# Performance work log

Measured on AMD Instinct MI355X. Metric: run time of the kernel, lower is better.

The kernel has to match this reference:

```python
import jax, jax.numpy as jnp
import numpy as np

B, N, C_IN, C_CH = 1, 512, 128, 128

def layer_norm(x, g, b, eps=1e-5):
    mu = jnp.mean(x, axis=-1, keepdims=True)
    var = jnp.var(x, axis=-1, keepdims=True)
    return (x - mu) * jax.lax.rsqrt(var + eps) * g + b

def setup_inputs() -> dict:
    key = jax.random.key(0)
    ks = jax.random.split(key, 16)
    s = 0.02
    # weights stored as [in, out] (torch Linear uses y = x @ W.T + b; we pre-transpose)
    return {
        "z": jax.random.normal(ks[0], (B, N, N, C_IN), jnp.float32),
        "mask": jax.random.randint(ks[1], (B, N, N), 0, 2).astype(bool),
        "g_in": jnp.ones((C_IN,), jnp.float32),
        "b_in": jnp.zeros((C_IN,), jnp.float32),
        "Wa": jax.random.normal(ks[2], (C_IN, C_CH), jnp.float32) * s,
        "ba": jnp.zeros((C_CH,), jnp.float32),
        "Wga": jax.random.normal(ks[3], (C_IN, C_CH), jnp.float32) * s,
        "bga": jax.random.normal(ks[4], (C_CH,), jnp.float32) * s,
        "Wb": jax.random.normal(ks[5], (C_IN, C_CH), jnp.float32) * s,
        "bb": jnp.zeros((C_CH,), jnp.float32),
        "Wgb": jax.random.normal(ks[6], (C_IN, C_CH), jnp.float32) * s,
        "bgb": jax.random.normal(ks[7], (C_CH,), jnp.float32) * s,
        "g_o": jnp.ones((C_CH,), jnp.float32),
        "b_o": jnp.zeros((C_CH,), jnp.float32),
        "Wgo": jax.random.normal(ks[8], (C_IN, C_IN), jnp.float32) * s,
        "bgo": jax.random.normal(ks[9], (C_IN,), jnp.float32) * s,
        "Wo": jax.random.normal(ks[10], (C_CH, C_IN), jnp.float32) * s,
        "bo": jnp.zeros((C_IN,), jnp.float32),
    }

def reference(z, mask, g_in, b_in, Wa, ba, Wga, bga, Wb, bb, Wgb, bgb,
              g_o, b_o, Wgo, bgo, Wo, bo):
    zn = layer_norm(z, g_in, b_in)                                  # [B,N,N,Cin]
    a = jax.nn.sigmoid(zn @ Wga + bga) * (zn @ Wa + ba)             # [B,N,N,Cch]
    b = jax.nn.sigmoid(zn @ Wgb + bgb) * (zn @ Wb + bb)
    m = mask[..., None]                                             # [B,N,N,1]
    a = jnp.where(m, 0.0, a)
    b = jnp.where(m, 0.0, b)
    # axis == 1: k[b,i,j,o] = sum_k a[b,i,k,o] * b[b,j,k,o]
    k = jnp.einsum('biko,bjko->bijo', a, b)
    return jax.nn.sigmoid(zn @ Wgo + bgo) * (layer_norm(k, g_o, b_o) @ Wo + bo)
```

## Files before the change

kernel.cpp:

```cpp
#include <hip/hip_runtime.h>

#define NDIM 512
#define CDIM 128
#define RDIM (NDIM * NDIM)

typedef __attribute__((ext_vector_type(8))) short bf16x8;
typedef __attribute__((ext_vector_type(8))) unsigned short ushort8;
typedef __attribute__((ext_vector_type(4))) float f32x4;

__device__ __forceinline__ float bf2f(unsigned short u) {
  union { unsigned int i; float f; } v; v.i = ((unsigned int)u) << 16; return v.f;
}
__device__ __forceinline__ unsigned short f2bf(float f) {
  union { float f; unsigned int i; } v; v.f = f;
  unsigned int r = v.i + 0x7fffu + ((v.i >> 16) & 1u);
  return (unsigned short)(r >> 16);
}
__device__ __forceinline__ float sigm(float x) { return 1.0f / (1.0f + __expf(-x)); }

__device__ __forceinline__ int sw(int row, int col) {
  return (row << 7) + ((((col >> 3) ^ (row & 7)) << 3) | (col & 7));
}

__global__ __launch_bounds__(256) void k0_prep(
    const float* __restrict__ Wga, const float* __restrict__ Wa,
    const float* __restrict__ Wgb, const float* __restrict__ Wb,
    const float* __restrict__ Wgo, const float* __restrict__ Wo,
    unsigned short* __restrict__ wsF) {
  const float* src;
  switch (blockIdx.x) {
    case 0: src = Wga; break;
    case 1: src = Wa;  break;
    case 2: src = Wgb; break;
    case 3: src = Wb;  break;
    case 4: src = Wgo; break;
    default: src = Wo; break;
  }
  const int t = threadIdx.x;
  unsigned short* dstF = wsF + blockIdx.x * 16384;
  for (int gid = t; gid < 2048; gid += 256) {
    const int fragid = gid >> 6, lane = gid & 63;
    const int kc = fragid >> 3, nf = fragid & 7;
    const int o = nf * 16 + (lane & 15);
    const int c0 = kc * 32 + (lane >> 4) * 8;
#pragma unroll
    for (int j = 0; j < 8; j++) dstF[gid * 8 + j] = f2bf(src[(c0 + j) * CDIM + o]);
  }
}

__device__ __forceinline__ bf16x8 ldfrag(const unsigned short* wf, int slot, int kc,
                                         int nf, int lane) {
  return *((const bf16x8*)(wf + (((slot * 32 + kc * 8 + nf) * 64 + lane) << 3)));
}

__global__ __launch_bounds__(256, 3) void k1_proj(
    const float* __restrict__ z, const int* __restrict__ mask,
    const float* __restrict__ g_in, const float* __restrict__ b_in,
    const float* __restrict__ bga, const float* __restrict__ ba,
    const float* __restrict__ bgb, const float* __restrict__ bb,
    const unsigned short* __restrict__ wf,
    unsigned short* __restrict__ a_t, unsigned short* __restrict__ b_t) {
  __shared__ unsigned short Xs[CDIM * CDIM];
  const int t = threadIdx.x;
  const int lane = t & 63;
  const int w = t >> 6;
  const int l15 = lane & 15, lq = lane >> 4;
  const int row0 = blockIdx.x * 128;

  {
    const int row = t >> 1, hf = t & 1;
    const float4* zp = (const float4*)(z + (size_t)(row0 + row) * CDIM + hf * 64);
    float s = 0.f, s2 = 0.f;
#pragma unroll
    for (int i = 0; i < 16; i++) {
      float4 x = zp[i];
      s += x.x + x.y + x.z + x.w;
      s2 += x.x * x.x + x.y * x.y + x.z * x.z + x.w * x.w;
    }
    s += __shfl_xor(s, 1);
    s2 += __shfl_xor(s2, 1);
    const float mean = s * 0.0078125f;
    const float var = s2 * 0.0078125f - mean * mean;
    const float rs = rsqrtf(var + 1e-5f);
    const float4* gp = (const float4*)(g_in + hf * 64);
    const float4* bp = (const float4*)(b_in + hf * 64);
#pragma unroll 4
    for (int u = 0; u < 8; u++) {
      float4 x0 = zp[2 * u], x1 = zp[2 * u + 1];
      float4 g0 = gp[2 * u], g1 = gp[2 * u + 1];
      float4 c0 = bp[2 * u], c1 = bp[2 * u + 1];
      ushort8 pk;
      pk[0] = f2bf((x0.x - mean) * rs * g0.x + c0.x);
      pk[1] = f2bf((x0.y - mean) * rs * g0.y + c0.y);
      pk[2] = f2bf((x0.z - mean) * rs * g0.z + c0.z);
      pk[3] = f2bf((x0.w - mean) * rs * g0.w + c0.w);
      pk[4] = f2bf((x1.x - mean) * rs * g1.x + c1.x);
      pk[5] = f2bf((x1.y - mean) * rs * g1.y + c1.y);
      pk[6] = f2bf((x1.z - mean) * rs * g1.z + c1.z);
      pk[7] = f2bf((x1.w - mean) * rs * g1.w + c1.w);
      const int su = (hf * 8 + u) ^ (row & 7);
      *((ushort8*)&Xs[(row << 7) + (su << 3)]) = pk;
    }
  }

  unsigned mbits = 0;
#pragma unroll
  for (int ms = 0; ms < 2; ms++)
#pragma unroll
    for (int r = 0; r < 4; r++) {
      const int rl = w * 32 + ms * 16 + (lq << 2) + r;
      if (mask[row0 + rl] != 0) mbits |= 1u << (ms * 4 + r);
    }

  __syncthreads();

  bf16x8 afr[2][4];
#pragma unroll
  for (int ms = 0; ms < 2; ms++) {
    const int m = w * 32 + ms * 16 + l15;
#pragma unroll
    for (int kc = 0; kc < 4; kc++)
      afr[ms][kc] = *((const bf16x8*)&Xs[sw(m, kc * 32 + (lq << 3))]);
  }
  __syncthreads();

  const f32x4 zv = {0.f, 0.f, 0.f, 0.f};

#pragma unroll 1
  for (int pair = 0; pair < 2; pair++) {
    const int sg = pair * 2, sv = pair * 2 + 1;
    const float* bgp = (pair == 0) ? bga : bgb;
    const float* bvp = (pair == 0) ? ba : bb;
#pragma unroll 1
    for (int half = 0; half < 2; half++) {
      f32x4 accg[2][4], accv[2][4];
#pragma unroll
      for (int i = 0; i < 2; i++)
#pragma unroll
        for (int j = 0; j < 4; j++) { accg[i][j] = zv; accv[i][j] = zv; }
#pragma unroll
      for (int kc = 0; kc < 4; kc++) {
#pragma unroll
        for (int nfh = 0; nfh < 4; nfh++) {
          const int fi = half * 4 + nfh;
          bf16x8 bg = ldfrag(wf, sg, kc, fi, lane);
          bf16x8 bv = ldfrag(wf, sv, kc, fi, lane);
          accg[0][nfh] = __builtin_amdgcn_mfma_f32_16x16x32_bf16(afr[0][kc], bg, accg[0][nfh], 0, 0, 0);
          accg[1][nfh] = __builtin_amdgcn_mfma_f32_16x16x32_bf16(afr[1][kc], bg, accg[1][nfh], 0, 0, 0);
          accv[0][nfh] = __builtin_amdgcn_mfma_f32_16x16x32_bf16(afr[0][kc], bv, accv[0][nfh], 0, 0, 0);
          accv[1][nfh] = __builtin_amdgcn_mfma_f32_16x16x32_bf16(afr[1][kc], bv, accv[1][nfh], 0, 0, 0);
        }
      }
#pragma unroll
      for (int ms = 0; ms < 2; ms++)
#pragma unroll
        for (int nfh = 0; nfh < 4; nfh++) {
          const int n = half * 64 + nfh * 16 + l15;
          const float bg = bgp[n], bv = bvp[n];
#pragma unroll
          for (int r = 0; r < 4; r++) {
            const int rl = w * 32 + ms * 16 + (lq << 2) + r;
            float val = sigm(accg[ms][nfh][r] + bg) * (accv[ms][nfh][r] + bv);
            if ((mbits >> (ms * 4 + r)) & 1u) val = 0.f;
            Xs[sw(n, rl)] = f2bf(val);
          }
        }
    }
    __syncthreads();
    unsigned short* dst = (pair == 0) ? a_t : b_t;
    {
      const int o = t >> 1, hf = t & 1;
#pragma unroll
      for (int u = 0; u < 8; u++) {
        const int ru = hf * 8 + u;
        const int su = ru ^ (o & 7);
        uint4 val = *((const uint4*)&Xs[(o << 7) + (su << 3)]);
        *((uint4*)&dst[(size_t)o * RDIM + row0 + ru * 8]) = val;
      }
    }
    __syncthreads();
  }
}

__global__ __launch_bounds__(256) void k2_einsum(
    const unsigned short* __restrict__ a_t, const unsigned short* __restrict__ b_t,
    unsigned short* __restrict__ k_t) {
  __shared__ unsigned short As[128 * 72];
  __shared__ unsigned short Bs[128 * 72];
  const int t = threadIdx.x;
  const int lane = t & 63;
  const int w = t >> 6;
  const int l15 = lane & 15, lq = lane >> 4;
  const int bid = (blockIdx.x & 7) * (2048 >> 3) + (blockIdx.x >> 3);
  const int o = bid >> 4;
  const int tile = bid & 15;
  const int i0 = (tile >> 2) * 128, j0 = (tile & 3) * 128;
  const size_t base = (size_t)o * RDIM;

  f32x4 acc[2][8];
  const f32x4 zv = {0.f, 0.f, 0.f, 0.f};
#pragma unroll
  for (int i = 0; i < 2; i++)
#pragma unroll
    for (int j = 0; j < 8; j++) acc[i][j] = zv;

  const int r = t & 127;
  const int isB = t >> 7;
  const unsigned short* srcp = (isB ? b_t : a_t) + base + (size_t)((isB ? j0 : i0) + r) * NDIM;
  unsigned short* dstp = isB ? &Bs[r * 72] : &As[r * 72];

  for (int k0 = 0; k0 < NDIM; k0 += 64) {
    __syncthreads();
    const uint4* s4 = (const uint4*)(srcp + k0);
#pragma unroll
    for (int u = 0; u < 8; u++) *((uint4*)&dstp[u * 8]) = s4[u];
    __syncthreads();
#pragma unroll
    for (int kc = 0; kc < 2; kc++) {
      const int kk = kc * 32 + (lq << 3);
      bf16x8 a0 = *((const bf16x8*)&As[(w * 32 + l15) * 72 + kk]);
      bf16x8 a1 = *((const bf16x8*)&As[(w * 32 + 16 + l15) * 72 + kk]);
#pragma unroll
      for (int nf = 0; nf < 8; nf++) {
        bf16x8 bfr = *((const bf16x8*)&Bs[(nf * 16 + l15) * 72 + kk]);
        acc[0][nf] = __builtin_amdgcn_mfma_f32_16x16x32_bf16(a0, bfr, acc[0][nf], 0, 0, 0);
        acc[1][nf] = __builtin_amdgcn_mfma_f32_16x16x32_bf16(a1, bfr, acc[1][nf], 0, 0, 0);
      }
    }
  }
#pragma unroll
  for (int ms = 0; ms < 2; ms++)
#pragma unroll
    for (int nf = 0; nf < 8; nf++)
#pragma unroll
      for (int r2 = 0; r2 < 4; r2++) {
        const int mi = i0 + w * 32 + ms * 16 + (lq << 2) + r2;
        const int nj = j0 + nf * 16 + l15;
        k_t[base + (size_t)mi * NDIM + nj] = f2bf(acc[ms][nf][r2]);
      }
}

__global__ __launch_bounds__(256, 2) void k3_final(
    const unsigned short* __restrict__ k_t, const unsigned short* __restrict__ wf,
    const float* __restrict__ z, const float* __restrict__ g_in,
    const float* __restrict__ b_in, const float* __restrict__ g_o,
    const float* __restrict__ b_o, const float* __restrict__ bgo,
    const float* __restrict__ bo, float* __restrict__ out) {
  __shared__ unsigned short Ks[CDIM * CDIM];
  __shared__ unsigned short XN[CDIM * CDIM];
  const int t = threadIdx.x;
  const int lane = t & 63;
  const int w = t >> 6;
  const int l15 = lane & 15, lq = lane >> 4;
  const int row0 = blockIdx.x * 128;

  {
    const int o = t >> 1, hf = t & 1;
    const uint4* src = (const uint4*)(k_t + (size_t)o * RDIM + row0 + hf * 64);
#pragma unroll
    for (int u = 0; u < 8; u++) {
      const int ru = hf * 8 + u;
      const int su = ru ^ (o & 7);
      *((uint4*)&Ks[(o << 7) + (su << 3)]) = src[u];
    }
  }
  {
    const int row = t >> 1, hf = t & 1;
    const float4* zp = (const float4*)(z + (size_t)(row0 + row) * CDIM + hf * 64);
    float s = 0.f, s2 = 0.f;
#pragma unroll
    for (int i = 0; i < 16; i++) {
      float4 x = zp[i];
      s += x.x + x.y + x.z + x.w;
      s2 += x.x * x.x + x.y * x.y + x.z * x.z + x.w * x.w;
    }
    s += __shfl_xor(s, 1);
    s2 += __shfl_xor(s2, 1);
    const float mean = s * 0.0078125f;
    const float var = s2 * 0.0078125f - mean * mean;
    const float rs = rsqrtf(var + 1e-5f);
    const float4* gp = (const float4*)(g_in + hf * 64);
    const float4* bp = (const float4*)(b_in + hf * 64);
#pragma unroll 4
    for (int u = 0; u < 8; u++) {
      float4 x0 = zp[2 * u], x1 = zp[2 * u + 1];
      float4 g0 = gp[2 * u], g1 = gp[2 * u + 1];
      float4 c0 = bp[2 * u], c1 = bp[2 * u + 1];
      ushort8 pk;
      pk[0] = f2bf((x0.x - mean) * rs * g0.x + c0.x);
      pk[1] = f2bf((x0.y - mean) * rs * g0.y + c0.y);
      pk[2] = f2bf((x0.z - mean) * rs * g0.z + c0.z);
      pk[3] = f2bf((x0.w - mean) * rs * g0.w + c0.w);
      pk[4] = f2bf((x1.x - mean) * rs * g1.x + c1.x);
      pk[5] = f2bf((x1.y - mean) * rs * g1.y + c1.y);
      pk[6] = f2bf((x1.z - mean) * rs * g1.z + c1.z);
      pk[7] = f2bf((x1.w - mean) * rs * g1.w + c1.w);
      const int su = (hf * 8 + u) ^ (row & 7);
      *((ushort8*)&XN[(row << 7) + (su << 3)]) = pk;
    }
  }
  __syncthreads();

  bf16x8 az[2][4];
#pragma unroll
  for (int ms = 0; ms < 2; ms++) {
    const int m = w * 32 + ms * 16 + l15;
#pragma unroll
    for (int kc = 0; kc < 4; kc++)
      az[ms][kc] = *((const bf16x8*)&XN[sw(m, kc * 32 + (lq << 3))]);
  }
  __syncthreads();

  {
    const int row = t >> 1, hf = t & 1;
    float x[64];
    float s = 0.f, s2 = 0.f;
#pragma unroll
    for (int i = 0; i < 64; i++) {
      x[i] = bf2f(Ks[sw(hf * 64 + i, row)]);
      s += x[i];
      s2 += x[i] * x[i];
    }
    s += __shfl_xor(s, 1);
    s2 += __shfl_xor(s2, 1);
    const float mean = s * 0.0078125f;
    const float var = s2 * 0.0078125f - mean * mean;
    const float rs = rsqrtf(var + 1e-5f);
#pragma unroll
    for (int i = 0; i < 64; i++) {
      const int o = hf * 64 + i;
      XN[sw(row, o)] = f2bf((x[i] - mean) * rs * g_o[o] + b_o[o]);
    }
  }
  __syncthreads();

  bf16x8 ak[2][4];
#pragma unroll
  for (int ms = 0; ms < 2; ms++) {
    const int m = w * 32 + ms * 16 + l15;
#pragma unroll
    for (int kc = 0; kc < 4; kc++)
      ak[ms][kc] = *((const bf16x8*)&XN[sw(m, kc * 32 + (lq << 3))]);
  }

  const f32x4 zv = {0.f, 0.f, 0.f, 0.f};
#pragma unroll 1
  for (int half = 0; half < 2; half++) {
    f32x4 accg[2][4], acco[2][4];
#pragma unroll
    for (int i = 0; i < 2; i++)
#pragma unroll
      for (int j = 0; j < 4; j++) { accg[i][j] = zv; acco[i][j] = zv; }
#pragma unroll
    for (int kc = 0; kc < 4; kc++) {
#pragma unroll
      for (int nfh = 0; nfh < 4; nfh++) {
        const int fi = half * 4 + nfh;
        bf16x8 bg = ldfrag(wf, 4, kc, fi, lane);
        bf16x8 bw = ldfrag(wf, 5, kc, fi, lane);
        accg[0][nfh] = __builtin_amdgcn_mfma_f32_16x16x32_bf16(az[0][kc], bg, accg[0][nfh], 0, 0, 0);
        accg[1][nfh] = __builtin_amdgcn_mfma_f32_16x16x32_bf16(az[1][kc], bg, accg[1][nfh], 0, 0, 0);
        acco[0][nfh] = __builtin_amdgcn_mfma_f32_16x16x32_bf16(ak[0][kc], bw, acco[0][nfh], 0, 0, 0);
        acco[1][nfh] = __builtin_amdgcn_mfma_f32_16x16x32_bf16(ak[1][kc], bw, acco[1][nfh], 0, 0, 0);
      }
    }
#pragma unroll
    for (int ms = 0; ms < 2; ms++)
#pragma unroll
      for (int nfh = 0; nfh < 4; nfh++) {
        const int n = half * 64 + nfh * 16 + l15;
        const float gb = bgo[n], ob = bo[n];
#pragma unroll
        for (int r = 0; r < 4; r++) {
          const int rl = w * 32 + ms * 16 + (lq << 2) + r;
          out[(size_t)(row0 + rl) * CDIM + n] =
              sigm(accg[ms][nfh][r] + gb) * (acco[ms][nfh][r] + ob);
        }
      }
  }
}

extern "C" void kernel_launch(void* const* d_in, const int* in_sizes, int n_in,
                              void* d_out, int out_size, void* d_ws, size_t ws_size,
                              hipStream_t stream) {
  const float* z    = (const float*)d_in[0];
  const int*   mask = (const int*)d_in[1];
  const float* g_in = (const float*)d_in[2];
  const float* b_in = (const float*)d_in[3];
  const float* Wa   = (const float*)d_in[4];
  const float* ba   = (const float*)d_in[5];
  const float* Wga  = (const float*)d_in[6];
  const float* bga  = (const float*)d_in[7];
  const float* Wb   = (const float*)d_in[8];
  const float* bb   = (const float*)d_in[9];
  const float* Wgb  = (const float*)d_in[10];
  const float* bgb  = (const float*)d_in[11];
  const float* g_o  = (const float*)d_in[12];
  const float* b_o  = (const float*)d_in[13];
  const float* Wgo  = (const float*)d_in[14];
  const float* bgo  = (const float*)d_in[15];
  const float* Wo   = (const float*)d_in[16];
  const float* bo   = (const float*)d_in[17];
  float* out = (float*)d_out;

  unsigned short* wsF = (unsigned short*)d_ws;
  unsigned short* a_t = wsF + 6 * (CDIM * CDIM);
  unsigned short* b_t = a_t + (size_t)CDIM * RDIM;
  unsigned short* k_t = b_t + (size_t)CDIM * RDIM;

  k0_prep<<<6, 256, 0, stream>>>(Wga, Wa, Wgb, Wb, Wgo, Wo, wsF);
  k1_proj<<<RDIM / 128, 256, 0, stream>>>(z, mask, g_in, b_in, bga, ba, bgb, bb,
                                          wsF, a_t, b_t);
  k2_einsum<<<CDIM * 16, 256, 0, stream>>>(a_t, b_t, k_t);
  k3_final<<<RDIM / 128, 256, 0, stream>>>(k_t, wsF, z, g_in, b_in, g_o, b_o,
                                           bgo, bo, out);
}
```

Before: 666.2 us.

## Restructure einsum kernel with 256x256 tiles and double-buffered direct-to-LDS loads

The batched einsum kernel moves from 128x128 tiles per 256-thread block to 256x256 tiles per 512-thread block, so each staged operand feeds more MFMAs. Global loads now go straight into LDS via global_load_lds with an XOR swizzle in place of padded rows. Two LDS buffers let the next k-slice load while the current one is computed. The cost is heavy LDS use (128KB) and many accumulator registers, giving one block per CU and only 512 blocks in the grid.

New measurement: 574.7 us. -13.7%, faster.

```diff
diff --git a/kernel.cpp b/kernel.cpp
--- a/kernel.cpp
+++ b/kernel.cpp
@@ -20,6 +20,12 @@
 
 __device__ __forceinline__ int sw(int row, int col) {
   return (row << 7) + ((((col >> 3) ^ (row & 7)) << 3) | (col & 7));
+}
+
+__device__ __forceinline__ void gld_lds16(const unsigned short* g, unsigned short* l) {
+  __builtin_amdgcn_global_load_lds(
+      (const __attribute__((address_space(1))) unsigned int*)g,
+      (__attribute__((address_space(3))) unsigned int*)l, 16, 0, 0);
 }
 
 __global__ __launch_bounds__(256) void k0_prep(
@@ -182,61 +188,82 @@
   }
 }
 
-__global__ __launch_bounds__(256) void k2_einsum(
+__global__ __launch_bounds__(512, 1) void k2_einsum(
     const unsigned short* __restrict__ a_t, const unsigned short* __restrict__ b_t,
     unsigned short* __restrict__ k_t) {
-  __shared__ unsigned short As[128 * 72];
-  __shared__ unsigned short Bs[128 * 72];
+  __shared__ unsigned short S[2][2][256 * 64];
   const int t = threadIdx.x;
   const int lane = t & 63;
-  const int w = t >> 6;
+  const int wid = t >> 6;
   const int l15 = lane & 15, lq = lane >> 4;
-  const int bid = (blockIdx.x & 7) * (2048 >> 3) + (blockIdx.x >> 3);
-  const int o = bid >> 4;
-  const int tile = bid & 15;
-  const int i0 = (tile >> 2) * 128, j0 = (tile & 3) * 128;
+  const int bid = (blockIdx.x & 7) * 64 + (blockIdx.x >> 3);
+  const int o = bid >> 2;
+  const int tile = bid & 3;
+  const int i0 = (tile >> 1) * 256, j0 = (tile & 1) * 256;
   const size_t base = (size_t)o * RDIM;
-
-  f32x4 acc[2][8];
+  const int wr = wid >> 2, wc = wid & 3;
+
+  const int srow = lane >> 3;
+  const int sgl = (lane & 7) ^ srow;
+
+  f32x4 acc[8][4];
   const f32x4 zv = {0.f, 0.f, 0.f, 0.f};
 #pragma unroll
-  for (int i = 0; i < 2; i++)
-#pragma unroll
-    for (int j = 0; j < 8; j++) acc[i][j] = zv;
-
-  const int r = t & 127;
-  const int isB = t >> 7;
-  const unsigned short* srcp = (isB ? b_t : a_t) + base + (size_t)((isB ? j0 : i0) + r) * NDIM;
-  unsigned short* dstp = isB ? &Bs[r * 72] : &As[r * 72];
-
-  for (int k0 = 0; k0 < NDIM; k0 += 64) {
+  for (int i = 0; i < 8; i++)
+#pragma unroll
+    for (int j = 0; j < 4; j++) acc[i][j] = zv;
+
+  auto stage = [&](int buf, int k0) {
+#pragma unroll
+    for (int c = 0; c < 4; c++) {
+      const int chunk = wid * 4 + c;
+      const int row = chunk * 8 + srow;
+      gld_lds16(a_t + base + (size_t)(i0 + row) * NDIM + k0 + sgl * 8,
+                &S[buf][0][chunk * 512]);
+      gld_lds16(b_t + base + (size_t)(j0 + row) * NDIM + k0 + sgl * 8,
+                &S[buf][1][chunk * 512]);
+    }
+  };
+
+  stage(0, 0);
+  __syncthreads();
+
+#pragma unroll 1
+  for (int ks = 0; ks < 8; ks++) {
+    const int cur = ks & 1;
+    if (ks < 7) stage(cur ^ 1, (ks + 1) * 64);
+    const unsigned short* Ab = &S[cur][0][0];
+    const unsigned short* Bb = &S[cur][1][0];
+#pragma unroll
+    for (int kc = 0; kc < 2; kc++) {
+      const int g = kc * 4 + lq;
+      bf16x8 bfr[4];
+#pragma unroll
+      for (int nf = 0; nf < 4; nf++) {
+        const int rb = wc * 64 + nf * 16 + l15;
+        bfr[nf] = *((const bf16x8*)&Bb[rb * 64 + ((g ^ (rb & 7)) << 3)]);
+      }
+#pragma unroll
+      for (int mf = 0; mf < 8; mf++) {
+        const int ra = wr * 128 + mf * 16 + l15;
+        bf16x8 af = *((const bf16x8*)&Ab[ra * 64 + ((g ^ (ra & 7)) << 3)]);
+#pragma unroll
+        for (int nf = 0; nf < 4; nf++)
+          acc[mf][nf] = __builtin_amdgcn_mfma_f32_16x16x32_bf16(af, bfr[nf], acc[mf][nf], 0, 0, 0);
+      }
+    }
     __syncthreads();
-    const uint4* s4 = (const uint4*)(srcp + k0);
-#pragma unroll
-    for (int u = 0; u < 8; u++) *((uint4*)&dstp[u * 8]) = s4[u];
-    __syncthreads();
-#pragma unroll
-    for (int kc = 0; kc < 2; kc++) {
-      const int kk = kc * 32 + (lq << 3);
-      bf16x8 a0 = *((const bf16x8*)&As[(w * 32 + l15) * 72 + kk]);
-      bf16x8 a1 = *((const bf16x8*)&As[(w * 32 + 16 + l15) * 72 + kk]);
-#pragma unroll
-      for (int nf = 0; nf < 8; nf++) {
-        bf16x8 bfr = *((const bf16x8*)&Bs[(nf * 16 + l15) * 72 + kk]);
-        acc[0][nf] = __builtin_amdgcn_mfma_f32_16x16x32_bf16(a0, bfr, acc[0][nf], 0, 0, 0);
-        acc[1][nf] = __builtin_amdgcn_mfma_f32_16x16x32_bf16(a1, bfr, acc[1][nf], 0, 0, 0);
-      }
-    }
-  }
-#pragma unroll
-  for (int ms = 0; ms < 2; ms++)
-#pragma unroll
-    for (int nf = 0; nf < 8; nf++)
+  }
+
+#pragma unroll
+  for (int mf = 0; mf < 8; mf++)
+#pragma unroll
+    for (int nf = 0; nf < 4; nf++)
 #pragma unroll
       for (int r2 = 0; r2 < 4; r2++) {
-        const int mi = i0 + w * 32 + ms * 16 + (lq << 2) + r2;
-        const int nj = j0 + nf * 16 + l15;
-        k_t[base + (size_t)mi * NDIM + nj] = f2bf(acc[ms][nf][r2]);
+        const int mi = i0 + wr * 128 + mf * 16 + (lq << 2) + r2;
+        const int nj = j0 + wc * 64 + nf * 16 + l15;
+        k_t[base + (size_t)mi * NDIM + nj] = f2bf(acc[mf][nf][r2]);
       }
 }
 
@@ -411,7 +438,7 @@
   k0_prep<<<6, 256, 0, stream>>>(Wga, Wa, Wgb, Wb, Wgo, Wo, wsF);
   k1_proj<<<RDIM / 128, 256, 0, stream>>>(z, mask, g_in, b_in, bga, ba, bgb, bb,
                                           wsF, a_t, b_t);
-  k2_einsum<<<CDIM * 16, 256, 0, stream>>>(a_t, b_t, k_t);
+  k2_einsum<<<512, 512, 0, stream>>>(a_t, b_t, k_t);
   k3_final<<<RDIM / 128, 256, 0, stream>>>(k_t, wsF, z, g_in, b_in, g_o, b_o,
                                            bgo, bo, out);
 }
```
